# Kernel optimization log

Hardware: AMD Instinct MI355X
Metric: run time of the kernel (lower is better)

## Reference

```python
import jax, jax.numpy as jnp
import numpy as np

N_NODES = 50000
N_EDGES = 1_600_000
IN_CH = 256
HEADS = 4
OUT_CH = 32


def setup_inputs() -> dict:
    key = jax.random.key(0)
    k1, k2, k3, k4 = jax.random.split(key, 4)
    x = jax.random.normal(k1, (N_NODES, IN_CH), dtype=jnp.float32)
    edge_index = jax.random.randint(k2, (2, N_EDGES), 0, N_NODES, dtype=jnp.int32)
    # xavier-uniform-like init scales
    W = jax.random.uniform(k3, (IN_CH, HEADS * OUT_CH), dtype=jnp.float32,
                           minval=-1.0, maxval=1.0) * np.sqrt(6.0 / (IN_CH + HEADS * OUT_CH))
    attn = jax.random.uniform(k4, (HEADS, 2 * OUT_CH), dtype=jnp.float32,
                              minval=-1.0, maxval=1.0) * np.sqrt(6.0 / (HEADS + 2 * OUT_CH))
    return {"x": x, "edge_index": edge_index, "W": W, "attn": attn}


def reference(x, edge_index, W, attn):
    n = x.shape[0]
    H = attn.shape[0]
    C = attn.shape[1] // 2
    # h = lin(x).view(n, H, C)
    h = (x @ W).reshape(n, H, C)
    row, col = edge_index[0], edge_index[1]
    # (cat([h_row, h_col]) * attn).sum(-1) == h_row.a_src + h_col.a_dst;
    # compute per-node scores then gather per edge (cheaper, same math).
    a_src, a_dst = attn[:, :C], attn[:, C:]
    s_src = jnp.einsum('nhc,hc->nh', h, a_src)  # [n, H]
    s_dst = jnp.einsum('nhc,hc->nh', h, a_dst)  # [n, H]
    alpha = jax.nn.leaky_relu(s_src[row] + s_dst[col], 0.2)  # [E, H]
    # segment softmax over edges grouped by target node `row`
    seg_max = jax.ops.segment_max(alpha, row, num_segments=n)  # [n, H]
    ex = jnp.exp(alpha - seg_max[row])
    denom = jax.ops.segment_sum(ex, row, num_segments=n)  # [n, H]
    alpha_norm = ex / denom[row]  # [E, H]
    # weighted scatter-add of source features (dropout p=0.0 is identity)
    out = jax.ops.segment_sum(alpha_norm[..., None] * h[col], row, num_segments=n)  # [n,H,C]
    return out.mean(axis=1), alpha_norm
```

## Files before the change

kernel.cpp:

```cpp
#include <hip/hip_runtime.h>

#define NNODES 50000
#define NEDGES 1600000
#define IN_CH 256
#define HEADS 4
#define OUT_CH 32
#define HC 128
#define NSB ((NNODES + 255) / 256)
#define NCHUNK 128
#define CE 12500
#define WORDS 25000

typedef unsigned int u32;
typedef unsigned short u16;
typedef short bf16x8 __attribute__((ext_vector_type(8)));
typedef u16 u16x8 __attribute__((ext_vector_type(8)));
typedef float f32x4 __attribute__((ext_vector_type(4)));

__device__ __forceinline__ float b2f(u16 s) { return __uint_as_float(((u32)s) << 16); }
__device__ __forceinline__ u16 f2b(float f) {
  u32 u = __float_as_uint(f);
  u32 r = (u + 0x7FFFu + ((u >> 16) & 1u)) >> 16;
  return (u16)r;
}
__device__ __forceinline__ float lrelu(float v) { return v >= 0.f ? v : 0.2f * v; }

__global__ __launch_bounds__(256) void k_wprep(const float* __restrict__ W,
                                               u16* __restrict__ wt) {
  int i = blockIdx.x * 256 + threadIdx.x;
  if (i >= IN_CH * HC) return;
  int kk = i & 31;
  int n = (i >> 5) & 127;
  int kt = i >> 12;
  wt[i] = f2b(W[(size_t)(kt * 32 + kk) * HC + n]);
}

__global__ __launch_bounds__(256) void k_gemm(const float* __restrict__ x,
                                              const u16* __restrict__ wt,
                                              const float* __restrict__ attn,
                                              u16* __restrict__ hb,
                                              float* __restrict__ s_src,
                                              float* __restrict__ s_dst) {
  __shared__ union {
    struct {
      u16 xh[64 * 32];
      u16 xl[64 * 32];
      u16 wh[128 * 32];
    } st;
    float cbuf[64 * 132];
  } L;
  __shared__ float sA[256];
  const int tid = threadIdx.x;
  const int wave = tid >> 6;
  const int lane = tid & 63;
  const int row0 = blockIdx.x * 64;
  sA[tid] = attn[tid];

  f32x4 acc[4][2] = {};
  const int frow = lane & 15;
  const int koff = (lane >> 4) << 4;

  const int sr = tid >> 2;
  const int skc = (tid & 3) << 3;
  const int sgrow = row0 + sr;
  const int sxb = (sr << 6) + (skc << 1);
  const int sxs = sxb ^ ((sr & 7) << 4);

  for (int kt = 0; kt < 8; ++kt) {
    {
      float4 v0 = make_float4(0.f, 0.f, 0.f, 0.f), v1 = v0;
      if (sgrow < NNODES) {
        const float* px = &x[(size_t)sgrow * IN_CH + kt * 32 + skc];
        v0 = *(const float4*)px;
        v1 = *(const float4*)(px + 4);
      }
      float vv[8] = {v0.x, v0.y, v0.z, v0.w, v1.x, v1.y, v1.z, v1.w};
      u16x8 hi, lo;
#pragma unroll
      for (int i = 0; i < 8; ++i) {
        u16 h = f2b(vv[i]);
        hi[i] = h;
        lo[i] = f2b(vv[i] - b2f(h));
      }
      *(u16x8*)((char*)L.st.xh + sxs) = hi;
      *(u16x8*)((char*)L.st.xl + sxs) = lo;
    }
#pragma unroll
    for (int li = 0; li < 2; ++li) {
      int i = tid + (li << 8);
      int col = i >> 2;
      int kb = (i & 3) << 4;
      u16x8 v = *(const u16x8*)((const char*)wt + (((size_t)(kt * 128 + col)) << 6) + kb);
      int sb = ((col << 6) + kb) ^ ((col & 7) << 4);
      *(u16x8*)((char*)L.st.wh + sb) = v;
    }
    __syncthreads();
    bf16x8 ah[4], al[4], bw[2];
#pragma unroll
    for (int mi = 0; mi < 4; ++mi) {
      int r = mi * 16 + frow;
      int sb = ((r << 6) + koff) ^ ((r & 7) << 4);
      ah[mi] = *(bf16x8*)((char*)L.st.xh + sb);
      al[mi] = *(bf16x8*)((char*)L.st.xl + sb);
    }
#pragma unroll
    for (int ni = 0; ni < 2; ++ni) {
      int c = (wave << 5) + ni * 16 + frow;
      int sb = ((c << 6) + koff) ^ ((c & 7) << 4);
      bw[ni] = *(bf16x8*)((char*)L.st.wh + sb);
    }
#pragma unroll
    for (int mi = 0; mi < 4; ++mi)
#pragma unroll
      for (int ni = 0; ni < 2; ++ni) {
        acc[mi][ni] = __builtin_amdgcn_mfma_f32_16x16x32_bf16(ah[mi], bw[ni], acc[mi][ni], 0, 0, 0);
        acc[mi][ni] = __builtin_amdgcn_mfma_f32_16x16x32_bf16(al[mi], bw[ni], acc[mi][ni], 0, 0, 0);
      }
    __syncthreads();
  }

#pragma unroll
  for (int mi = 0; mi < 4; ++mi)
#pragma unroll
    for (int ni = 0; ni < 2; ++ni) {
#pragma unroll
      for (int reg = 0; reg < 4; ++reg) {
        int row = mi * 16 + ((lane >> 4) << 2) + reg;
        int col = (wave << 5) + (ni << 4) + frow;
        L.cbuf[row * 132 + col] = acc[mi][ni][reg];
      }
    }
  __syncthreads();

  const int tc = tid & 31;
  const int tr = tid >> 5;
  const int head = tc >> 3;
  const int cb = (tc & 7) << 2;
  const float4 as4 = *(const float4*)&sA[head * 64 + cb];
  const float4 ad4 = *(const float4*)&sA[head * 64 + 32 + cb];
#pragma unroll
  for (int i = 0; i < 8; ++i) {
    int row = (tr << 3) + i;
    int grow = row0 + row;
    float4 v = *(const float4*)&L.cbuf[row * 132 + (tc << 2)];
    float ps = v.x * as4.x + v.y * as4.y + v.z * as4.z + v.w * as4.w;
    float pd = v.x * ad4.x + v.y * ad4.y + v.z * ad4.z + v.w * ad4.w;
    ps += __shfl_xor(ps, 1); ps += __shfl_xor(ps, 2); ps += __shfl_xor(ps, 4);
    pd += __shfl_xor(pd, 1); pd += __shfl_xor(pd, 2); pd += __shfl_xor(pd, 4);
    if (grow < NNODES) {
      u16 q[4] = {f2b(v.x), f2b(v.y), f2b(v.z), f2b(v.w)};
      *(ushort4*)&hb[(size_t)grow * HC + (tc << 2)] = *(ushort4*)q;
      if ((tc & 7) == 0) {
        s_src[(size_t)grow * 4 + head] = ps;
        s_dst[(size_t)grow * 4 + head] = pd;
      }
    }
  }
}

__global__ __launch_bounds__(256) void k_chist(const int* __restrict__ rowi,
                                               u32* __restrict__ chunk_hist,
                                               u16* __restrict__ lslot) {
  __shared__ u32 lh[WORDS];
  const int c = blockIdx.x;
  const int tid = threadIdx.x;
  for (int i = tid; i < WORDS; i += 256) lh[i] = 0;
  __syncthreads();
  const int base = c * CE;
  for (int i = tid; i < CE; i += 256) {
    int e = base + i;
    int r = rowi[e];
    u32 sh = (u32)(r & 1) << 4;
    u32 old = atomicAdd(&lh[r >> 1], 1u << sh);
    lslot[e] = (u16)((old >> sh) & 0xFFFFu);
  }
  __syncthreads();
  u32* dst = chunk_hist + (size_t)c * WORDS;
  for (int i = tid; i < WORDS; i += 256) dst[i] = lh[i];
}

__global__ __launch_bounds__(256) void k_cscan(u32* __restrict__ chunk_hist,
                                               int* __restrict__ counts) {
  __shared__ u32 tile[NCHUNK][64];
  const int w0 = blockIdx.x * 64;
  const int tid = threadIdx.x;
  for (int i = tid; i < NCHUNK * 64; i += 256) {
    int c = i >> 6, wl = i & 63;
    int w = w0 + wl;
    tile[c][wl] = (w < WORDS) ? chunk_hist[(size_t)c * WORDS + w] : 0u;
  }
  __syncthreads();
  if (tid < 64) {
    u32 slo = 0, shi = 0;
    for (int c = 0; c < NCHUNK; ++c) {
      u32 v = tile[c][tid];
      tile[c][tid] = slo | (shi << 16);
      slo += v & 0xFFFFu;
      shi += v >> 16;
    }
    int w = w0 + tid;
    if (w < WORDS) {
      int r = w << 1;
      if (r < NNODES) counts[r] = (int)slo;
      if (r + 1 < NNODES) counts[r + 1] = (int)shi;
    }
  }
  __syncthreads();
  for (int i = tid; i < NCHUNK * 64; i += 256) {
    int c = i >> 6, wl = i & 63;
    int w = w0 + wl;
    if (w < WORDS) chunk_hist[(size_t)c * WORDS + w] = tile[c][wl];
  }
}

__global__ __launch_bounds__(256) void k_scan1(const int* __restrict__ counts,
                                               int* __restrict__ bsum) {
  int i = blockIdx.x * 256 + threadIdx.x;
  int v = (i < NNODES) ? counts[i] : 0;
#pragma unroll
  for (int m = 1; m < 64; m <<= 1) v += __shfl_xor(v, m);
  __shared__ int ws[4];
  if ((threadIdx.x & 63) == 0) ws[threadIdx.x >> 6] = v;
  __syncthreads();
  if (threadIdx.x == 0) bsum[blockIdx.x] = ws[0] + ws[1] + ws[2] + ws[3];
}

__global__ __launch_bounds__(256) void k_scan2(const int* __restrict__ bsum,
                                               int* __restrict__ boff) {
  __shared__ int s[256];
  int t = threadIdx.x;
  int v = (t < NSB) ? bsum[t] : 0;
  s[t] = v;
  __syncthreads();
  for (int off = 1; off < 256; off <<= 1) {
    int u = (t >= off) ? s[t - off] : 0;
    __syncthreads();
    s[t] += u;
    __syncthreads();
  }
  boff[t] = s[t] - v;
}

__global__ __launch_bounds__(256) void k_scan3(const int* __restrict__ counts,
                                               const int* __restrict__ boff,
                                               int* __restrict__ row_ptr) {
  __shared__ int s[256];
  int t = threadIdx.x;
  int i = blockIdx.x * 256 + t;
  int v = (i < NNODES) ? counts[i] : 0;
  s[t] = v;
  __syncthreads();
  for (int off = 1; off < 256; off <<= 1) {
    int u = (t >= off) ? s[t - off] : 0;
    __syncthreads();
    s[t] += u;
    __syncthreads();
  }
  if (i < NNODES) row_ptr[i] = boff[blockIdx.x] + s[t] - v;
  if (i == 0) row_ptr[NNODES] = NEDGES;
}

__global__ void k_scatter(const int* __restrict__ rowi, const int* __restrict__ coli,
                          const int* __restrict__ row_ptr,
                          const u32* __restrict__ chunk_hist,
                          const u16* __restrict__ lslot,
                          int* __restrict__ col_csr, int* __restrict__ eid_csr) {
  int e = blockIdx.x * 256 + threadIdx.x;
  if (e >= NEDGES) return;
  int r = rowi[e];
  int c = e / CE;
  u32 word = chunk_hist[(size_t)c * WORDS + (r >> 1)];
  int off = (int)((word >> ((u32)(r & 1) << 4)) & 0xFFFFu);
  int pos = row_ptr[r] + off + (int)lslot[e];
  col_csr[pos] = coli[e];
  eid_csr[pos] = e;
}

__global__ __launch_bounds__(256) void k_softmax(const int* __restrict__ col_csr,
                                                 const int* __restrict__ eid_csr,
                                                 const int* __restrict__ row_ptr,
                                                 const float* __restrict__ s_src,
                                                 const float* __restrict__ s_dst,
                                                 float* __restrict__ alpha_out,
                                                 u16* __restrict__ an16) {
  const int wid = threadIdx.x >> 6;
  const int lane = threadIdx.x & 63;
  const int r = blockIdx.x * 4 + wid;
  if (r >= NNODES) return;
  const int p0 = row_ptr[r], p1 = row_ptr[r + 1];
  const int deg = p1 - p0;
  if (deg == 0) return;
  const float4 ss = *(const float4*)&s_src[(size_t)r * 4];
  const float NEG = -3.0e38f;

  if (deg <= 64) {
    int e = 0;
    float4 al = make_float4(NEG, NEG, NEG, NEG);
    if (lane < deg) {
      int c = col_csr[p0 + lane];
      e = eid_csr[p0 + lane];
      float4 sd = *(const float4*)&s_dst[(size_t)c * 4];
      al.x = lrelu(ss.x + sd.x);
      al.y = lrelu(ss.y + sd.y);
      al.z = lrelu(ss.z + sd.z);
      al.w = lrelu(ss.w + sd.w);
    }
    float4 mx = al;
#pragma unroll
    for (int m = 1; m < 64; m <<= 1) {
      mx.x = fmaxf(mx.x, __shfl_xor(mx.x, m));
      mx.y = fmaxf(mx.y, __shfl_xor(mx.y, m));
      mx.z = fmaxf(mx.z, __shfl_xor(mx.z, m));
      mx.w = fmaxf(mx.w, __shfl_xor(mx.w, m));
    }
    float4 ex = make_float4(0.f, 0.f, 0.f, 0.f);
    if (lane < deg) {
      ex.x = __expf(al.x - mx.x);
      ex.y = __expf(al.y - mx.y);
      ex.z = __expf(al.z - mx.z);
      ex.w = __expf(al.w - mx.w);
    }
    float4 sm = ex;
#pragma unroll
    for (int m = 1; m < 64; m <<= 1) {
      sm.x += __shfl_xor(sm.x, m);
      sm.y += __shfl_xor(sm.y, m);
      sm.z += __shfl_xor(sm.z, m);
      sm.w += __shfl_xor(sm.w, m);
    }
    if (lane < deg) {
      float4 an = make_float4(ex.x / sm.x, ex.y / sm.y, ex.z / sm.z, ex.w / sm.w);
      *(float4*)&alpha_out[(size_t)e * 4] = an;
      u16 q[4] = {f2b(an.x), f2b(an.y), f2b(an.z), f2b(an.w)};
      *(ushort4*)&an16[(size_t)(p0 + lane) * 4] = *(ushort4*)q;
    }
  } else {
    float4 mx = make_float4(NEG, NEG, NEG, NEG);
    for (int p = p0 + lane; p < p1; p += 64) {
      int c = col_csr[p];
      float4 sd = *(const float4*)&s_dst[(size_t)c * 4];
      mx.x = fmaxf(mx.x, lrelu(ss.x + sd.x));
      mx.y = fmaxf(mx.y, lrelu(ss.y + sd.y));
      mx.z = fmaxf(mx.z, lrelu(ss.z + sd.z));
      mx.w = fmaxf(mx.w, lrelu(ss.w + sd.w));
    }
#pragma unroll
    for (int m = 1; m < 64; m <<= 1) {
      mx.x = fmaxf(mx.x, __shfl_xor(mx.x, m));
      mx.y = fmaxf(mx.y, __shfl_xor(mx.y, m));
      mx.z = fmaxf(mx.z, __shfl_xor(mx.z, m));
      mx.w = fmaxf(mx.w, __shfl_xor(mx.w, m));
    }
    float4 sm = make_float4(0.f, 0.f, 0.f, 0.f);
    for (int p = p0 + lane; p < p1; p += 64) {
      int c = col_csr[p];
      float4 sd = *(const float4*)&s_dst[(size_t)c * 4];
      sm.x += __expf(lrelu(ss.x + sd.x) - mx.x);
      sm.y += __expf(lrelu(ss.y + sd.y) - mx.y);
      sm.z += __expf(lrelu(ss.z + sd.z) - mx.z);
      sm.w += __expf(lrelu(ss.w + sd.w) - mx.w);
    }
#pragma unroll
    for (int m = 1; m < 64; m <<= 1) {
      sm.x += __shfl_xor(sm.x, m);
      sm.y += __shfl_xor(sm.y, m);
      sm.z += __shfl_xor(sm.z, m);
      sm.w += __shfl_xor(sm.w, m);
    }
    float4 rd = make_float4(1.f / sm.x, 1.f / sm.y, 1.f / sm.z, 1.f / sm.w);
    for (int p = p0 + lane; p < p1; p += 64) {
      int c = col_csr[p];
      int e = eid_csr[p];
      float4 sd = *(const float4*)&s_dst[(size_t)c * 4];
      float4 an;
      an.x = __expf(lrelu(ss.x + sd.x) - mx.x) * rd.x;
      an.y = __expf(lrelu(ss.y + sd.y) - mx.y) * rd.y;
      an.z = __expf(lrelu(ss.z + sd.z) - mx.z) * rd.z;
      an.w = __expf(lrelu(ss.w + sd.w) - mx.w) * rd.w;
      *(float4*)&alpha_out[(size_t)e * 4] = an;
      u16 q[4] = {f2b(an.x), f2b(an.y), f2b(an.z), f2b(an.w)};
      *(ushort4*)&an16[(size_t)p * 4] = *(ushort4*)q;
    }
  }
}

__global__ __launch_bounds__(256) void k_aggr(const int* __restrict__ col_csr,
                                              const int* __restrict__ row_ptr,
                                              const u16* __restrict__ an16,
                                              const u16* __restrict__ hb,
                                              float* __restrict__ out_mean) {
  const int wid = threadIdx.x >> 6;
  const int lane = threadIdx.x & 63;
  const int r = blockIdx.x * 4 + wid;
  if (r >= NNODES) return;
  const int p0 = row_ptr[r], p1 = row_ptr[r + 1];
  const int half = lane >> 5;
  const int sl = lane & 31;
  const int hd = sl >> 3;
  const int boff = sl << 3;
  float a0 = 0.f, a1 = 0.f, a2 = 0.f, a3 = 0.f;

  int p = p0;
  for (; p + 16 <= p1; p += 16) {
    int cs[8];
    float wv[8];
    u32 h0[8], h1[8];
#pragma unroll
    for (int i = 0; i < 8; ++i) {
      int idx = p + (i << 1) + half;
      cs[i] = col_csr[idx];
      wv[i] = b2f(an16[(size_t)idx * 4 + hd]);
    }
#pragma unroll
    for (int i = 0; i < 8; ++i) {
      const u32* hp = (const u32*)((const char*)hb + ((size_t)cs[i] << 8) + boff);
      h0[i] = hp[0];
      h1[i] = hp[1];
    }
#pragma unroll
    for (int i = 0; i < 8; ++i) {
      a0 += wv[i] * __uint_as_float(h0[i] << 16);
      a1 += wv[i] * __uint_as_float(h0[i] & 0xFFFF0000u);
      a2 += wv[i] * __uint_as_float(h1[i] << 16);
      a3 += wv[i] * __uint_as_float(h1[i] & 0xFFFF0000u);
    }
  }
  for (; p < p1; p += 2) {
    int idx = p + half;
    bool act = idx < p1;
    int c = act ? col_csr[idx] : 0;
    float w = act ? b2f(an16[(size_t)idx * 4 + hd]) : 0.f;
    const u32* hp = (const u32*)((const char*)hb + ((size_t)c << 8) + boff);
    u32 x0 = hp[0], x1 = hp[1];
    a0 += w * __uint_as_float(x0 << 16);
    a1 += w * __uint_as_float(x0 & 0xFFFF0000u);
    a2 += w * __uint_as_float(x1 << 16);
    a3 += w * __uint_as_float(x1 & 0xFFFF0000u);
  }
  a0 += __shfl_xor(a0, 32); a1 += __shfl_xor(a1, 32);
  a2 += __shfl_xor(a2, 32); a3 += __shfl_xor(a3, 32);
  a0 += __shfl_xor(a0, 8);  a1 += __shfl_xor(a1, 8);
  a2 += __shfl_xor(a2, 8);  a3 += __shfl_xor(a3, 8);
  a0 += __shfl_xor(a0, 16); a1 += __shfl_xor(a1, 16);
  a2 += __shfl_xor(a2, 16); a3 += __shfl_xor(a3, 16);
  if (lane < 8) {
    float4 o = make_float4(a0 * 0.25f, a1 * 0.25f, a2 * 0.25f, a3 * 0.25f);
    *(float4*)&out_mean[(size_t)r * 32 + (lane << 2)] = o;
  }
}

extern "C" void kernel_launch(void* const* d_in, const int* in_sizes, int n_in,
                              void* d_out, int out_size, void* d_ws, size_t ws_size,
                              hipStream_t stream) {
  const float* x = (const float*)d_in[0];
  const int* ei = (const int*)d_in[1];
  const float* W = (const float*)d_in[2];
  const float* attn = (const float*)d_in[3];
  const int* rowi = ei;
  const int* coli = ei + NEDGES;

  float* out_mean = (float*)d_out;
  float* alpha_out = (float*)d_out + (size_t)NNODES * 32;

  char* w = (char*)d_ws;
  u16* hb = (u16*)w;          w += (size_t)NNODES * HC * 2;
  u16* an16 = (u16*)w;        w += (size_t)NEDGES * 4 * 2;
  float* s_src = (float*)w;   w += (size_t)NNODES * 4 * 4;
  float* s_dst = (float*)w;   w += (size_t)NNODES * 4 * 4;
  int* counts = (int*)w;      w += (size_t)NNODES * 4;
  int* bsum = (int*)w;        w += (size_t)256 * 4;
  int* boff = (int*)w;        w += (size_t)256 * 4;
  int* row_ptr = (int*)w;     w += (size_t)50016 * 4;
  u16* lslot = (u16*)w;       w += (size_t)NEDGES * 2;
  int* col_csr = (int*)w;     w += (size_t)NEDGES * 4;
  int* eid_csr = (int*)w;     w += (size_t)NEDGES * 4;
  u32* chunk_hist = (u32*)w;  w += (size_t)NCHUNK * WORDS * 4;
  u16* wt = (u16*)w;          w += (size_t)IN_CH * HC * 2;

  k_wprep<<<(IN_CH * HC + 255) / 256, 256, 0, stream>>>(W, wt);
  k_gemm<<<(NNODES + 63) / 64, 256, 0, stream>>>(x, wt, attn, hb, s_src, s_dst);
  k_chist<<<NCHUNK, 256, 0, stream>>>(rowi, chunk_hist, lslot);
  k_cscan<<<(WORDS + 63) / 64, 256, 0, stream>>>(chunk_hist, counts);
  k_scan1<<<NSB, 256, 0, stream>>>(counts, bsum);
  k_scan2<<<1, 256, 0, stream>>>(bsum, boff);
  k_scan3<<<NSB, 256, 0, stream>>>(counts, boff, row_ptr);
  k_scatter<<<(NEDGES + 255) / 256, 256, 0, stream>>>(rowi, coli, row_ptr, chunk_hist, lslot, col_csr, eid_csr);
  k_softmax<<<(NNODES + 3) / 4, 256, 0, stream>>>(col_csr, eid_csr, row_ptr, s_src, s_dst, alpha_out, an16);
  k_aggr<<<(NNODES + 3) / 4, 256, 0, stream>>>(col_csr, row_ptr, an16, hb, out_mean);
}
```

Before: 232.5 us.

## Write alpha in edge order via per-node softmax stats and compact CSR

Softmax now stores each node's max and reciprocal denominator in a packed 16-float node record, alongside the source and destination scores. A new edge-ordered kernel recomputes the normalized alpha from that record and writes it with coalesced stores, replacing the scattered float4 writes indexed by edge id. This removes the eid_csr array entirely, and col_csr shrinks to 16-bit indices, which fits because the node count is below 65536. The cost is an extra kernel that re-reads row and col indices and gathers node records per edge, plus recomputing exp for every edge.

```diff
diff --git a/kernel.cpp b/kernel.cpp
--- a/kernel.cpp
+++ b/kernel.cpp
@@ -25,6 +25,8 @@
 }
 __device__ __forceinline__ float lrelu(float v) { return v >= 0.f ? v : 0.2f * v; }
 
+#define NR 16
+
 __global__ __launch_bounds__(256) void k_wprep(const float* __restrict__ W,
                                                u16* __restrict__ wt) {
   int i = blockIdx.x * 256 + threadIdx.x;
@@ -39,8 +41,7 @@
                                               const u16* __restrict__ wt,
                                               const float* __restrict__ attn,
                                               u16* __restrict__ hb,
-                                              float* __restrict__ s_src,
-                                              float* __restrict__ s_dst) {
+                                              float* __restrict__ nrec) {
   __shared__ union {
     struct {
       u16 xh[64 * 32];
@@ -151,8 +152,8 @@
       u16 q[4] = {f2b(v.x), f2b(v.y), f2b(v.z), f2b(v.w)};
       *(ushort4*)&hb[(size_t)grow * HC + (tc << 2)] = *(ushort4*)q;
       if ((tc & 7) == 0) {
-        s_src[(size_t)grow * 4 + head] = ps;
-        s_dst[(size_t)grow * 4 + head] = pd;
+        nrec[(size_t)grow * NR + head] = ps;
+        nrec[(size_t)grow * NR + 4 + head] = pd;
       }
     }
   }
@@ -264,7 +265,7 @@
                           const int* __restrict__ row_ptr,
                           const u32* __restrict__ chunk_hist,
                           const u16* __restrict__ lslot,
-                          int* __restrict__ col_csr, int* __restrict__ eid_csr) {
+                          u16* __restrict__ col_csr) {
   int e = blockIdx.x * 256 + threadIdx.x;
   if (e >= NEDGES) return;
   int r = rowi[e];
@@ -272,16 +273,12 @@
   u32 word = chunk_hist[(size_t)c * WORDS + (r >> 1)];
   int off = (int)((word >> ((u32)(r & 1) << 4)) & 0xFFFFu);
   int pos = row_ptr[r] + off + (int)lslot[e];
-  col_csr[pos] = coli[e];
-  eid_csr[pos] = e;
-}
-
-__global__ __launch_bounds__(256) void k_softmax(const int* __restrict__ col_csr,
-                                                 const int* __restrict__ eid_csr,
+  col_csr[pos] = (u16)coli[e];
+}
+
+__global__ __launch_bounds__(256) void k_softmax(const u16* __restrict__ col_csr,
                                                  const int* __restrict__ row_ptr,
-                                                 const float* __restrict__ s_src,
-                                                 const float* __restrict__ s_dst,
-                                                 float* __restrict__ alpha_out,
+                                                 float* __restrict__ nrec,
                                                  u16* __restrict__ an16) {
   const int wid = threadIdx.x >> 6;
   const int lane = threadIdx.x & 63;
@@ -290,16 +287,14 @@
   const int p0 = row_ptr[r], p1 = row_ptr[r + 1];
   const int deg = p1 - p0;
   if (deg == 0) return;
-  const float4 ss = *(const float4*)&s_src[(size_t)r * 4];
+  const float4 ss = *(const float4*)&nrec[(size_t)r * NR];
   const float NEG = -3.0e38f;
 
   if (deg <= 64) {
-    int e = 0;
     float4 al = make_float4(NEG, NEG, NEG, NEG);
     if (lane < deg) {
       int c = col_csr[p0 + lane];
-      e = eid_csr[p0 + lane];
-      float4 sd = *(const float4*)&s_dst[(size_t)c * 4];
+      float4 sd = *(const float4*)&nrec[(size_t)c * NR + 4];
       al.x = lrelu(ss.x + sd.x);
       al.y = lrelu(ss.y + sd.y);
       al.z = lrelu(ss.z + sd.z);
@@ -328,17 +323,20 @@
       sm.z += __shfl_xor(sm.z, m);
       sm.w += __shfl_xor(sm.w, m);
     }
+    float4 rd = make_float4(1.f / sm.x, 1.f / sm.y, 1.f / sm.z, 1.f / sm.w);
+    if (lane == 0) {
+      *(float4*)&nrec[(size_t)r * NR + 8] = mx;
+      *(float4*)&nrec[(size_t)r * NR + 12] = rd;
+    }
     if (lane < deg) {
-      float4 an = make_float4(ex.x / sm.x, ex.y / sm.y, ex.z / sm.z, ex.w / sm.w);
-      *(float4*)&alpha_out[(size_t)e * 4] = an;
-      u16 q[4] = {f2b(an.x), f2b(an.y), f2b(an.z), f2b(an.w)};
+      u16 q[4] = {f2b(ex.x * rd.x), f2b(ex.y * rd.y), f2b(ex.z * rd.z), f2b(ex.w * rd.w)};
       *(ushort4*)&an16[(size_t)(p0 + lane) * 4] = *(ushort4*)q;
     }
   } else {
     float4 mx = make_float4(NEG, NEG, NEG, NEG);
     for (int p = p0 + lane; p < p1; p += 64) {
       int c = col_csr[p];
-      float4 sd = *(const float4*)&s_dst[(size_t)c * 4];
+      float4 sd = *(const float4*)&nrec[(size_t)c * NR + 4];
       mx.x = fmaxf(mx.x, lrelu(ss.x + sd.x));
       mx.y = fmaxf(mx.y, lrelu(ss.y + sd.y));
       mx.z = fmaxf(mx.z, lrelu(ss.z + sd.z));
@@ -354,7 +352,7 @@
     float4 sm = make_float4(0.f, 0.f, 0.f, 0.f);
     for (int p = p0 + lane; p < p1; p += 64) {
       int c = col_csr[p];
-      float4 sd = *(const float4*)&s_dst[(size_t)c * 4];
+      float4 sd = *(const float4*)&nrec[(size_t)c * NR + 4];
       sm.x += __expf(lrelu(ss.x + sd.x) - mx.x);
       sm.y += __expf(lrelu(ss.y + sd.y) - mx.y);
       sm.z += __expf(lrelu(ss.z + sd.z) - mx.z);
@@ -368,23 +366,44 @@
       sm.w += __shfl_xor(sm.w, m);
     }
     float4 rd = make_float4(1.f / sm.x, 1.f / sm.y, 1.f / sm.z, 1.f / sm.w);
+    if (lane == 0) {
+      *(float4*)&nrec[(size_t)r * NR + 8] = mx;
+      *(float4*)&nrec[(size_t)r * NR + 12] = rd;
+    }
     for (int p = p0 + lane; p < p1; p += 64) {
       int c = col_csr[p];
-      int e = eid_csr[p];
-      float4 sd = *(const float4*)&s_dst[(size_t)c * 4];
-      float4 an;
-      an.x = __expf(lrelu(ss.x + sd.x) - mx.x) * rd.x;
-      an.y = __expf(lrelu(ss.y + sd.y) - mx.y) * rd.y;
-      an.z = __expf(lrelu(ss.z + sd.z) - mx.z) * rd.z;
-      an.w = __expf(lrelu(ss.w + sd.w) - mx.w) * rd.w;
-      *(float4*)&alpha_out[(size_t)e * 4] = an;
-      u16 q[4] = {f2b(an.x), f2b(an.y), f2b(an.z), f2b(an.w)};
+      float4 sd = *(const float4*)&nrec[(size_t)c * NR + 4];
+      float4 ex;
+      ex.x = __expf(lrelu(ss.x + sd.x) - mx.x) * rd.x;
+      ex.y = __expf(lrelu(ss.y + sd.y) - mx.y) * rd.y;
+      ex.z = __expf(lrelu(ss.z + sd.z) - mx.z) * rd.z;
+      ex.w = __expf(lrelu(ss.w + sd.w) - mx.w) * rd.w;
+      u16 q[4] = {f2b(ex.x), f2b(ex.y), f2b(ex.z), f2b(ex.w)};
       *(ushort4*)&an16[(size_t)p * 4] = *(ushort4*)q;
     }
   }
 }
 
-__global__ __launch_bounds__(256) void k_aggr(const int* __restrict__ col_csr,
+__global__ void k_alphaf(const int* __restrict__ rowi, const int* __restrict__ coli,
+                         const float* __restrict__ nrec,
+                         float* __restrict__ alpha_out) {
+  int e = blockIdx.x * 256 + threadIdx.x;
+  if (e >= NEDGES) return;
+  int r = rowi[e], c = coli[e];
+  const float* nr = &nrec[(size_t)r * NR];
+  float4 ss = *(const float4*)(nr);
+  float4 m4 = *(const float4*)(nr + 8);
+  float4 rd = *(const float4*)(nr + 12);
+  float4 sd = *(const float4*)&nrec[(size_t)c * NR + 4];
+  float4 an;
+  an.x = __expf(lrelu(ss.x + sd.x) - m4.x) * rd.x;
+  an.y = __expf(lrelu(ss.y + sd.y) - m4.y) * rd.y;
+  an.z = __expf(lrelu(ss.z + sd.z) - m4.z) * rd.z;
+  an.w = __expf(lrelu(ss.w + sd.w) - m4.w) * rd.w;
+  *(float4*)&alpha_out[(size_t)e * 4] = an;
+}
+
+__global__ __launch_bounds__(256) void k_aggr(const u16* __restrict__ col_csr,
                                               const int* __restrict__ row_ptr,
                                               const u16* __restrict__ an16,
                                               const u16* __restrict__ hb,
@@ -428,7 +447,7 @@
   for (; p < p1; p += 2) {
     int idx = p + half;
     bool act = idx < p1;
-    int c = act ? col_csr[idx] : 0;
+    int c = act ? (int)col_csr[idx] : 0;
     float w = act ? b2f(an16[(size_t)idx * 4 + hd]) : 0.f;
     const u32* hp = (const u32*)((const char*)hb + ((size_t)c << 8) + boff);
     u32 x0 = hp[0], x1 = hp[1];
@@ -465,26 +484,25 @@
   char* w = (char*)d_ws;
   u16* hb = (u16*)w;          w += (size_t)NNODES * HC * 2;
   u16* an16 = (u16*)w;        w += (size_t)NEDGES * 4 * 2;
-  float* s_src = (float*)w;   w += (size_t)NNODES * 4 * 4;
-  float* s_dst = (float*)w;   w += (size_t)NNODES * 4 * 4;
+  float* nrec = (float*)w;    w += (size_t)NNODES * NR * 4;
   int* counts = (int*)w;      w += (size_t)NNODES * 4;
   int* bsum = (int*)w;        w += (size_t)256 * 4;
   int* boff = (int*)w;        w += (size_t)256 * 4;
   int* row_ptr = (int*)w;     w += (size_t)50016 * 4;
   u16* lslot = (u16*)w;       w += (size_t)NEDGES * 2;
-  int* col_csr = (int*)w;     w += (size_t)NEDGES * 4;
-  int* eid_csr = (int*)w;     w += (size_t)NEDGES * 4;
+  u16* col_csr = (u16*)w;     w += (size_t)NEDGES * 2;
   u32* chunk_hist = (u32*)w;  w += (size_t)NCHUNK * WORDS * 4;
   u16* wt = (u16*)w;          w += (size_t)IN_CH * HC * 2;
 
   k_wprep<<<(IN_CH * HC + 255) / 256, 256, 0, stream>>>(W, wt);
-  k_gemm<<<(NNODES + 63) / 64, 256, 0, stream>>>(x, wt, attn, hb, s_src, s_dst);
+  k_gemm<<<(NNODES + 63) / 64, 256, 0, stream>>>(x, wt, attn, hb, nrec);
   k_chist<<<NCHUNK, 256, 0, stream>>>(rowi, chunk_hist, lslot);
   k_cscan<<<(WORDS + 63) / 64, 256, 0, stream>>>(chunk_hist, counts);
   k_scan1<<<NSB, 256, 0, stream>>>(counts, bsum);
   k_scan2<<<1, 256, 0, stream>>>(bsum, boff);
   k_scan3<<<NSB, 256, 0, stream>>>(counts, boff, row_ptr);
-  k_scatter<<<(NEDGES + 255) / 256, 256, 0, stream>>>(rowi, coli, row_ptr, chunk_hist, lslot, col_csr, eid_csr);
-  k_softmax<<<(NNODES + 3) / 4, 256, 0, stream>>>(col_csr, eid_csr, row_ptr, s_src, s_dst, alpha_out, an16);
+  k_scatter<<<(NEDGES + 255) / 256, 256, 0, stream>>>(rowi, coli, row_ptr, chunk_hist, lslot, col_csr);
+  k_softmax<<<(NNODES + 3) / 4, 256, 0, stream>>>(col_csr, row_ptr, nrec, an16);
+  k_alphaf<<<(NEDGES + 255) / 256, 256, 0, stream>>>(rowi, coli, nrec, alpha_out);
   k_aggr<<<(NNODES + 3) / 4, 256, 0, stream>>>(col_csr, row_ptr, an16, hb, out_mean);
 }
```

Result: no change. 230.1 us (-1.1%).
